# Kernel tuning notes

Measured on AMD Instinct MI355X. Metric: run time of the kernel, lower is better.

Reference implementation:

```python
import jax, jax.numpy as jnp
import numpy as np

V, E, H, L, B = 32000, 128, 32, 64, 32


def setup_inputs() -> dict:
    key = jax.random.key(0)
    k0, k1, k2, k3, k4, k5 = jax.random.split(key, 6)
    stdv = 1.0 / np.sqrt(H)
    we = jax.random.uniform(k0, (V, E), minval=-stdv, maxval=stdv, dtype=jnp.float32)
    we = we.at[1].set(0.0)  # pad token row zeroed, as in original
    i2h1 = jax.random.uniform(k1, (E + H, H), minval=-stdv, maxval=stdv, dtype=jnp.float32)
    i2h2 = jax.random.uniform(k2, (E + H, H), minval=-stdv, maxval=stdv, dtype=jnp.float32)
    h2o = jax.random.uniform(k3, (2 * H, V), minval=-stdv, maxval=stdv, dtype=jnp.float32)
    bias = jnp.ones((1, H), dtype=jnp.float32)  # assigned after reset_parameters -> stays ones
    hidden_init = jax.random.normal(k4, (1, H), dtype=jnp.float32)  # plain buffer, not reset
    inp = jax.random.randint(k5, (L, B), 0, V, dtype=jnp.int64)
    return {"inp": inp, "we": we, "i2h1": i2h1, "i2h2": i2h2,
            "h2o": h2o, "bias": bias, "hidden_init": hidden_init}


def reference(inp, we, i2h1, i2h2, h2o, bias, hidden_init):
    Lr, Br = inp.shape
    Hh = hidden_init.shape[1]
    emb = we[inp]                                   # [L,B,E] embedding gather
    h0 = jnp.broadcast_to(hidden_init, (Br, Hh))    # [B,H]
    b = jnp.broadcast_to(bias, (Br, Hh))            # [B,H]

    def make_step(W):
        def step(h, e):
            h_new = jnp.tanh(jnp.concatenate([e, h], axis=1) @ W + b)
            return h_new, h_new
        return step

    # forward direction: hf[i] = hidden after consuming token i
    _, hf = jax.lax.scan(make_step(i2h1), h0, emb)
    # backward direction (scan over reversed time, flip back)
    _, hb_rev = jax.lax.scan(make_step(i2h2), h0, emb[::-1])
    hb = hb_rev[::-1]                               # hb[i] = bwd hidden after token i

    # original uses hiddenf[i] (pre-token-i fwd state) and hiddenb[i+1] (post-token-(i+1) bwd state)
    hf_used = jnp.concatenate([h0[None], hf[:-1]], axis=0)   # [L,B,H]
    hb_used = jnp.concatenate([hb[1:], h0[None]], axis=0)    # [L,B,H]

    hcat = jnp.concatenate([hf_used, hb_used], axis=-1)      # [L,B,2H]
    logits = jnp.einsum('lbh,hv->lbv', hcat, h2o)            # [L,B,V]
    return jax.nn.log_softmax(logits, axis=-1)
```

## Files before the change

kernel.cpp:

```cpp
#include <hip/hip_runtime.h>
#include <hip/hip_cooperative_groups.h>

namespace cg = cooperative_groups;

#define V_SZ 32000
#define E_SZ 128
#define H_SZ 32
#define L_SZ 64
#define B_SZ 32
#define M_TOT 2048
#define K2 64
#define NVT 125

typedef __bf16 bf16x8 __attribute__((ext_vector_type(8)));
typedef float f32x4 __attribute__((ext_vector_type(4)));

__device__ __forceinline__ unsigned short f2bf(float f) {
    unsigned int u = __float_as_uint(f);
    u += 0x7FFFu + ((u >> 16) & 1u);
    return (unsigned short)(u >> 16);
}

__device__ __forceinline__ void load_vfrag(
    const __bf16* __restrict__ h2oT, int vbase, int lg, int lr,
    bf16x8 vf[4][2]) {
#pragma unroll
    for (int i = 0; i < 4; ++i) {
        const __bf16* vp = h2oT + (size_t)(vbase + i * 16 + lr) * K2 + lg * 8;
        vf[i][0] = *(const bf16x8*)(vp);
        vf[i][1] = *(const bf16x8*)(vp + 32);
    }
}

__device__ __forceinline__ void load_hfrag(
    const __bf16* __restrict__ hcat, int rowbase, int lg, int lr,
    bf16x8 hf[4][2]) {
#pragma unroll
    for (int j = 0; j < 4; ++j) {
        const __bf16* hp = hcat + (size_t)(rowbase + j * 16 + lr) * K2 + lg * 8;
        hf[j][0] = *(const bf16x8*)(hp);
        hf[j][1] = *(const bf16x8*)(hp + 32);
    }
}

__device__ __forceinline__ void tile_gemm_t(
    const bf16x8 vf[4][2], const bf16x8 hf[4][2], f32x4 acc[4][4]) {
#pragma unroll
    for (int i = 0; i < 4; ++i)
#pragma unroll
        for (int j = 0; j < 4; ++j) acc[i][j] = (f32x4){0.f, 0.f, 0.f, 0.f};
#pragma unroll
    for (int i = 0; i < 4; ++i)
#pragma unroll
        for (int j = 0; j < 4; ++j) {
            acc[i][j] = __builtin_amdgcn_mfma_f32_16x16x32_bf16(vf[i][0], hf[j][0], acc[i][j], 0, 0, 0);
            acc[i][j] = __builtin_amdgcn_mfma_f32_16x16x32_bf16(vf[i][1], hf[j][1], acc[i][j], 0, 0, 0);
        }
}

template <typename EP>
__device__ __forceinline__ void sweep8(
    const __bf16* __restrict__ hcat, int y0, int lg, int lr, EP&& ep) {
    bf16x8 hfA[4][2], hfB[4][2];
    load_hfrag(hcat, y0, lg, lr, hfA);
#pragma unroll
    for (int t = 0; t < 8; ++t) {
        if (t & 1) {
            if (t < 7) load_hfrag(hcat, y0 + (t + 1) * 64, lg, lr, hfA);
            ep(hfB, y0 + t * 64);
        } else {
            if (t < 7) load_hfrag(hcat, y0 + (t + 1) * 64, lg, lr, hfB);
            ep(hfA, y0 + t * 64);
        }
    }
}

struct EpA {
    const bf16x8 (*vf)[2];
    float* S;
    int lane, lg, lr;
    __device__ __forceinline__ void operator()(const bf16x8 hf[4][2], int rowbase) const {
        f32x4 acc[4][4];
        tile_gemm_t((const bf16x8(*)[2])vf, hf, acc);
        float srow[4];
#pragma unroll
        for (int j = 0; j < 4; ++j) {
            float s = 0.f;
#pragma unroll
            for (int i = 0; i < 4; ++i)
#pragma unroll
                for (int r = 0; r < 4; ++r) s += __expf(acc[i][j][r]);
            srow[j] = s;
        }
#pragma unroll
        for (int j = 0; j < 4; ++j) {
            srow[j] += __shfl_xor(srow[j], 16, 64);
            srow[j] += __shfl_xor(srow[j], 32, 64);
        }
        if (lane < 16) {
#pragma unroll
            for (int j = 0; j < 4; ++j)
                atomicAdd(&S[rowbase + j * 16 + lane], srow[j]);
        }
    }
};

struct EpB {
    const bf16x8 (*vf)[2];
    const float* S;
    float* out;
    int vbase, lg, lr;
    __device__ __forceinline__ void operator()(const bf16x8 hf[4][2], int rowbase) const {
        float lsev[4];
#pragma unroll
        for (int j = 0; j < 4; ++j)
            lsev[j] = logf(S[rowbase + j * 16 + lr]);
        f32x4 acc[4][4];
        tile_gemm_t((const bf16x8(*)[2])vf, hf, acc);
#pragma unroll
        for (int j = 0; j < 4; ++j) {
            float* rp = out + (size_t)(rowbase + j * 16 + lr) * V_SZ + vbase + lg * 4;
#pragma unroll
            for (int i = 0; i < 4; ++i) {
                f32x4 v;
                v.x = acc[i][j].x - lsev[j];
                v.y = acc[i][j].y - lsev[j];
                v.z = acc[i][j].z - lsev[j];
                v.w = acc[i][j].w - lsev[j];
                *(f32x4*)(rp + i * 16) = v;
            }
        }
    }
};

__global__ __launch_bounds__(256) void k_prep_rnn(
    const int* __restrict__ inp, const float* __restrict__ we,
    const float* __restrict__ i2h1, const float* __restrict__ i2h2,
    const float* __restrict__ h2o, const float* __restrict__ bias,
    const float* __restrict__ hinit,
    unsigned short* __restrict__ hcat_u, unsigned short* __restrict__ h2oT_u,
    float* __restrict__ S) {
    const int tid = threadIdx.x;
    const int p = blockIdx.x;
    if (p < 500) {
        if (p == 0) {
#pragma unroll
            for (int i = tid; i < M_TOT; i += 256) S[i] = 0.f;
        }
        const int v = p * 64 + (tid & 63);
        const int kg = tid >> 6;
        unsigned int* dst = (unsigned int*)(h2oT_u + (size_t)v * K2 + kg * 16);
#pragma unroll
        for (int kk = 0; kk < 16; kk += 2) {
            const int k = kg * 16 + kk;
            float a = h2o[(size_t)k * V_SZ + v];
            float b = h2o[(size_t)(k + 1) * V_SZ + v];
            dst[kk >> 1] = (unsigned int)f2bf(a) | ((unsigned int)f2bf(b) << 16);
        }
        return;
    }
    const int w2 = p - 500;
    const int dir = w2 >> 4;
    const int bpair = w2 & 15;
    const float* W = dir ? i2h2 : i2h1;
    __shared__ float Xl[L_SZ * 2 * H_SZ];
    {
        const int j = tid & 31, bb = (tid >> 5) & 1, to = tid >> 6;
        const int b = bpair * 2 + bb;
        const float bj = bias[j];
        for (int tt = 0; tt < 16; ++tt) {
            const int t = to * 16 + tt;
            const int idx = inp[t * B_SZ + b];
            const float* er = we + (size_t)idx * E_SZ;
            float acc = bj;
#pragma unroll
            for (int k0 = 0; k0 < E_SZ; k0 += 4) {
                f32x4 e4 = *(const f32x4*)(er + k0);
                acc += e4.x * W[(k0 + 0) * H_SZ + j];
                acc += e4.y * W[(k0 + 1) * H_SZ + j];
                acc += e4.z * W[(k0 + 2) * H_SZ + j];
                acc += e4.w * W[(k0 + 3) * H_SZ + j];
            }
            Xl[(t * 2 + bb) * H_SZ + j] = acc;
        }
    }
    __syncthreads();
    if (tid < 64) {
        const int lane = tid;
        const int bb = lane >> 5;
        const int b = bpair * 2 + bb;
        const int j = lane & 31;
        const int srcbase = lane & 32;
        float wh[H_SZ];
#pragma unroll
        for (int k = 0; k < H_SZ; ++k) wh[k] = W[(E_SZ + k) * H_SZ + j];
        float h = hinit[j];
        for (int step = 0; step < L_SZ; ++step) {
            const int tt = dir ? (L_SZ - 1 - step) : step;
            hcat_u[(tt * B_SZ + b) * K2 + dir * H_SZ + j] = f2bf(h);
            float a0 = Xl[(tt * 2 + bb) * H_SZ + j];
            float a1 = 0.f, a2 = 0.f, a3 = 0.f;
#pragma unroll
            for (int k = 0; k < H_SZ; k += 4) {
                a0 += __shfl(h, srcbase | k, 64) * wh[k];
                a1 += __shfl(h, srcbase | (k + 1), 64) * wh[k + 1];
                a2 += __shfl(h, srcbase | (k + 2), 64) * wh[k + 2];
                a3 += __shfl(h, srcbase | (k + 3), 64) * wh[k + 3];
            }
            float x2 = (a0 + a1) + (a2 + a3);
            float e = __expf(2.f * x2);
            h = 1.f - 2.f * __builtin_amdgcn_rcpf(e + 1.f);
        }
    }
}

__global__ __launch_bounds__(256) void k_fused(
    const unsigned short* __restrict__ hcat_u,
    const unsigned short* __restrict__ h2oT_u,
    float* __restrict__ S, float* __restrict__ out) {
    cg::grid_group gg = cg::this_grid();
    const int tid = threadIdx.x;
    const int wave = tid >> 6, lane = tid & 63;
    const int lg = lane >> 4, lr = lane & 15;
    const int xcol = blockIdx.x >> 2;
    const int y0 = (blockIdx.x & 3) * 512;
    const int vbase = xcol * 256 + wave * 64;
    const __bf16* hcat = (const __bf16*)hcat_u;
    const __bf16* h2oT = (const __bf16*)h2oT_u;

    bf16x8 vf[4][2];
    load_vfrag(h2oT, vbase, lg, lr, vf);

    EpA epa{vf, S, lane, lg, lr};
    sweep8(hcat, y0, lg, lr, epa);

    __threadfence();
    gg.sync();

    EpB epb{vf, S, out, vbase, lg, lr};
    sweep8(hcat, y0, lg, lr, epb);
}

__global__ __launch_bounds__(256) void k_pass_a(
    const __bf16* __restrict__ hcat, const __bf16* __restrict__ h2oT,
    float* __restrict__ S) {
    const int tid = threadIdx.x;
    const int wave = tid >> 6, lane = tid & 63;
    const int lg = lane >> 4, lr = lane & 15;
    const int y0 = blockIdx.y * 512;
    const int vbase = blockIdx.x * 256 + wave * 64;
    bf16x8 vf[4][2];
    load_vfrag(h2oT, vbase, lg, lr, vf);
    EpA epa{vf, S, lane, lg, lr};
    sweep8(hcat, y0, lg, lr, epa);
}

__global__ __launch_bounds__(256) void k_pass_b(
    const __bf16* __restrict__ hcat, const __bf16* __restrict__ h2oT,
    const float* __restrict__ S, float* __restrict__ out) {
    const int tid = threadIdx.x;
    const int wave = tid >> 6, lane = tid & 63;
    const int lg = lane >> 4, lr = lane & 15;
    const int y0 = blockIdx.y * 512;
    const int vbase = blockIdx.x * 256 + wave * 64;
    bf16x8 vf[4][2];
    load_vfrag(h2oT, vbase, lg, lr, vf);
    EpB epb{vf, S, out, vbase, lg, lr};
    sweep8(hcat, y0, lg, lr, epb);
}

extern "C" void kernel_launch(void* const* d_in, const int* in_sizes, int n_in,
                              void* d_out, int out_size, void* d_ws, size_t ws_size,
                              hipStream_t stream) {
    (void)in_sizes; (void)n_in; (void)out_size; (void)ws_size;
    const int*   inp   = (const int*)d_in[0];
    const float* we    = (const float*)d_in[1];
    const float* i2h1  = (const float*)d_in[2];
    const float* i2h2  = (const float*)d_in[3];
    const float* h2o   = (const float*)d_in[4];
    const float* bias  = (const float*)d_in[5];
    const float* hinit = (const float*)d_in[6];
    float* out = (float*)d_out;
    char* ws = (char*)d_ws;
    unsigned short* hcat_u = (unsigned short*)(ws);
    unsigned short* h2oT_u = (unsigned short*)(ws + 262144);
    float*          S      = (float*)(ws + 4358144);

    k_prep_rnn<<<532, 256, 0, stream>>>(inp, we, i2h1, i2h2, h2o, bias, hinit,
                                        hcat_u, h2oT_u, S);

    hipError_t e = hipErrorUnknown;
    int occ = 0;
    if (hipOccupancyMaxActiveBlocksPerMultiprocessor(&occ, k_fused, 256, 0)
            == hipSuccess && occ * 256 >= 500) {
        void* args[] = {(void*)&hcat_u, (void*)&h2oT_u, (void*)&S, (void*)&out};
        e = hipLaunchCooperativeKernel((void*)k_fused, dim3(500), dim3(256),
                                       args, 0, stream);
    }
    if (e != hipSuccess) {
        k_pass_a<<<dim3(NVT, 4), 256, 0, stream>>>(
            (const __bf16*)hcat_u, (const __bf16*)h2oT_u, S);
        k_pass_b<<<dim3(NVT, 4), 256, 0, stream>>>(
            (const __bf16*)hcat_u, (const __bf16*)h2oT_u, S, out);
    }
}
```

Before: 154.1 us.

## Fold prep/RNN into cooperative kernel and double grid with half-height row tiles

Moves the h2o transpose, RNN recurrence and S zeroing into the cooperative fused kernel behind an extra grid sync, removing a separate kernel launch. It also doubles the cooperative grid to 1000 blocks (launch_bounds 256,4), with each block sweeping 256 rows instead of 512, which spreads the GEMM and log-softmax work over more CUs. In exchange there is one more grid-wide barrier, the serial RNN blocks now sit on the critical path inside the fused kernel, and each block reloads its h2o fragments for half as much reuse.

```diff
diff --git a/kernel.cpp b/kernel.cpp
--- a/kernel.cpp
+++ b/kernel.cpp
@@ -11,6 +11,7 @@
 #define M_TOT 2048
 #define K2 64
 #define NVT 125
+#define GRID_F 1000
 
 typedef __bf16 bf16x8 __attribute__((ext_vector_type(8)));
 typedef float f32x4 __attribute__((ext_vector_type(4)));
@@ -59,26 +60,23 @@
 }
 
 template <typename EP>
-__device__ __forceinline__ void sweep8(
+__device__ __forceinline__ void sweep4(
     const __bf16* __restrict__ hcat, int y0, int lg, int lr, EP&& ep) {
     bf16x8 hfA[4][2], hfB[4][2];
     load_hfrag(hcat, y0, lg, lr, hfA);
-#pragma unroll
-    for (int t = 0; t < 8; ++t) {
-        if (t & 1) {
-            if (t < 7) load_hfrag(hcat, y0 + (t + 1) * 64, lg, lr, hfA);
-            ep(hfB, y0 + t * 64);
-        } else {
-            if (t < 7) load_hfrag(hcat, y0 + (t + 1) * 64, lg, lr, hfB);
-            ep(hfA, y0 + t * 64);
-        }
-    }
+    load_hfrag(hcat, y0 + 64, lg, lr, hfB);
+    ep(hfA, y0);
+    load_hfrag(hcat, y0 + 128, lg, lr, hfA);
+    ep(hfB, y0 + 64);
+    load_hfrag(hcat, y0 + 192, lg, lr, hfB);
+    ep(hfA, y0 + 128);
+    ep(hfB, y0 + 192);
 }
 
 struct EpA {
     const bf16x8 (*vf)[2];
     float* S;
-    int lane, lg, lr;
+    int lane;
     __device__ __forceinline__ void operator()(const bf16x8 hf[4][2], int rowbase) const {
         f32x4 acc[4][4];
         tile_gemm_t((const bf16x8(*)[2])vf, hf, acc);
@@ -133,37 +131,29 @@
     }
 };
 
-__global__ __launch_bounds__(256) void k_prep_rnn(
-    const int* __restrict__ inp, const float* __restrict__ we,
-    const float* __restrict__ i2h1, const float* __restrict__ i2h2,
-    const float* __restrict__ h2o, const float* __restrict__ bias,
-    const float* __restrict__ hinit,
-    unsigned short* __restrict__ hcat_u, unsigned short* __restrict__ h2oT_u,
-    float* __restrict__ S) {
-    const int tid = threadIdx.x;
-    const int p = blockIdx.x;
-    if (p < 500) {
-        if (p == 0) {
-#pragma unroll
-            for (int i = tid; i < M_TOT; i += 256) S[i] = 0.f;
-        }
-        const int v = p * 64 + (tid & 63);
-        const int kg = tid >> 6;
-        unsigned int* dst = (unsigned int*)(h2oT_u + (size_t)v * K2 + kg * 16);
-#pragma unroll
-        for (int kk = 0; kk < 16; kk += 2) {
-            const int k = kg * 16 + kk;
-            float a = h2o[(size_t)k * V_SZ + v];
-            float b = h2o[(size_t)(k + 1) * V_SZ + v];
-            dst[kk >> 1] = (unsigned int)f2bf(a) | ((unsigned int)f2bf(b) << 16);
-        }
-        return;
-    }
-    const int w2 = p - 500;
+__device__ __forceinline__ void transpose_unit(
+    int p, int tid, const float* __restrict__ h2o,
+    unsigned short* __restrict__ h2oT_u) {
+    const int v = p * 64 + (tid & 63);
+    const int kg = tid >> 6;
+    unsigned int* dst = (unsigned int*)(h2oT_u + (size_t)v * K2 + kg * 16);
+#pragma unroll
+    for (int kk = 0; kk < 16; kk += 2) {
+        const int k = kg * 16 + kk;
+        float a = h2o[(size_t)k * V_SZ + v];
+        float b = h2o[(size_t)(k + 1) * V_SZ + v];
+        dst[kk >> 1] = (unsigned int)f2bf(a) | ((unsigned int)f2bf(b) << 16);
+    }
+}
+
+__device__ __forceinline__ void rnn_unit(
+    int w2, int tid, float* Xl, const int* __restrict__ inp,
+    const float* __restrict__ we, const float* __restrict__ i2h1,
+    const float* __restrict__ i2h2, const float* __restrict__ bias,
+    const float* __restrict__ hinit, unsigned short* __restrict__ hcat_u) {
     const int dir = w2 >> 4;
     const int bpair = w2 & 15;
     const float* W = dir ? i2h2 : i2h1;
-    __shared__ float Xl[L_SZ * 2 * H_SZ];
     {
         const int j = tid & 31, bb = (tid >> 5) & 1, to = tid >> 6;
         const int b = bpair * 2 + bb;
@@ -214,31 +204,65 @@
     }
 }
 
-__global__ __launch_bounds__(256) void k_fused(
-    const unsigned short* __restrict__ hcat_u,
-    const unsigned short* __restrict__ h2oT_u,
+__global__ __launch_bounds__(256, 4) void k_fused(
+    const int* __restrict__ inp, const float* __restrict__ we,
+    const float* __restrict__ i2h1, const float* __restrict__ i2h2,
+    const float* __restrict__ h2o, const float* __restrict__ bias,
+    const float* __restrict__ hinit,
+    unsigned short* __restrict__ hcat_u, unsigned short* __restrict__ h2oT_u,
     float* __restrict__ S, float* __restrict__ out) {
     cg::grid_group gg = cg::this_grid();
+    __shared__ float Xl[L_SZ * 2 * H_SZ];
     const int tid = threadIdx.x;
+    const int p = blockIdx.x;
     const int wave = tid >> 6, lane = tid & 63;
     const int lg = lane >> 4, lr = lane & 15;
-    const int xcol = blockIdx.x >> 2;
-    const int y0 = (blockIdx.x & 3) * 512;
-    const int vbase = xcol * 256 + wave * 64;
+
+    if (p < 500) {
+        transpose_unit(p, tid, h2o, h2oT_u);
+    } else if (p < 532) {
+        rnn_unit(p - 500, tid, Xl, inp, we, i2h1, i2h2, bias, hinit, hcat_u);
+    } else if (p == 532) {
+        for (int i = tid; i < M_TOT; i += 256) S[i] = 0.f;
+    }
+    __threadfence();
+    gg.sync();
+
     const __bf16* hcat = (const __bf16*)hcat_u;
     const __bf16* h2oT = (const __bf16*)h2oT_u;
+    const int xcol = p >> 3;
+    const int y0 = (p & 7) * 256;
+    const int vbase = xcol * 256 + wave * 64;
 
     bf16x8 vf[4][2];
     load_vfrag(h2oT, vbase, lg, lr, vf);
 
-    EpA epa{vf, S, lane, lg, lr};
-    sweep8(hcat, y0, lg, lr, epa);
-
+    EpA epa{vf, S, lane};
+    sweep4(hcat, y0, lg, lr, epa);
     __threadfence();
     gg.sync();
 
     EpB epb{vf, S, out, vbase, lg, lr};
-    sweep8(hcat, y0, lg, lr, epb);
+    sweep4(hcat, y0, lg, lr, epb);
+}
+
+__global__ __launch_bounds__(256) void k_prep_rnn(
+    const int* __restrict__ inp, const float* __restrict__ we,
+    const float* __restrict__ i2h1, const float* __restrict__ i2h2,
+    const float* __restrict__ h2o, const float* __restrict__ bias,
+    const float* __restrict__ hinit,
+    unsigned short* __restrict__ hcat_u, unsigned short* __restrict__ h2oT_u,
+    float* __restrict__ S) {
+    __shared__ float Xl[L_SZ * 2 * H_SZ];
+    const int tid = threadIdx.x;
+    const int p = blockIdx.x;
+    if (p < 500) {
+        if (p == 0)
+            for (int i = tid; i < M_TOT; i += 256) S[i] = 0.f;
+        transpose_unit(p, tid, h2o, h2oT_u);
+        return;
+    }
+    rnn_unit(p - 500, tid, Xl, inp, we, i2h1, i2h2, bias, hinit, hcat_u);
 }
 
 __global__ __launch_bounds__(256) void k_pass_a(
@@ -247,12 +271,12 @@
     const int tid = threadIdx.x;
     const int wave = tid >> 6, lane = tid & 63;
     const int lg = lane >> 4, lr = lane & 15;
-    const int y0 = blockIdx.y * 512;
+    const int y0 = blockIdx.y * 256;
     const int vbase = blockIdx.x * 256 + wave * 64;
     bf16x8 vf[4][2];
     load_vfrag(h2oT, vbase, lg, lr, vf);
-    EpA epa{vf, S, lane, lg, lr};
-    sweep8(hcat, y0, lg, lr, epa);
+    EpA epa{vf, S, lane};
+    sweep4(hcat, y0, lg, lr, epa);
 }
 
 __global__ __launch_bounds__(256) void k_pass_b(
@@ -261,12 +285,12 @@
     const int tid = threadIdx.x;
     const int wave = tid >> 6, lane = tid & 63;
     const int lg = lane >> 4, lr = lane & 15;
-    const int y0 = blockIdx.y * 512;
+    const int y0 = blockIdx.y * 256;
     const int vbase = blockIdx.x * 256 + wave * 64;
     bf16x8 vf[4][2];
     load_vfrag(h2oT, vbase, lg, lr, vf);
     EpB epb{vf, S, out, vbase, lg, lr};
-    sweep8(hcat, y0, lg, lr, epb);
+    sweep4(hcat, y0, lg, lr, epb);
 }
 
 extern "C" void kernel_launch(void* const* d_in, const int* in_sizes, int n_in,
@@ -286,21 +310,23 @@
     unsigned short* h2oT_u = (unsigned short*)(ws + 262144);
     float*          S      = (float*)(ws + 4358144);
 
-    k_prep_rnn<<<532, 256, 0, stream>>>(inp, we, i2h1, i2h2, h2o, bias, hinit,
-                                        hcat_u, h2oT_u, S);
-
     hipError_t e = hipErrorUnknown;
     int occ = 0;
     if (hipOccupancyMaxActiveBlocksPerMultiprocessor(&occ, k_fused, 256, 0)
-            == hipSuccess && occ * 256 >= 500) {
-        void* args[] = {(void*)&hcat_u, (void*)&h2oT_u, (void*)&S, (void*)&out};
-        e = hipLaunchCooperativeKernel((void*)k_fused, dim3(500), dim3(256),
+            == hipSuccess && occ * 256 >= GRID_F) {
+        void* args[] = {
+            (void*)&inp, (void*)&we, (void*)&i2h1, (void*)&i2h2, (void*)&h2o,
+            (void*)&bias, (void*)&hinit, (void*)&hcat_u, (void*)&h2oT_u,
+            (void*)&S, (void*)&out};
+        e = hipLaunchCooperativeKernel((void*)k_fused, dim3(GRID_F), dim3(256),
                                        args, 0, stream);
     }
     if (e != hipSuccess) {
-        k_pass_a<<<dim3(NVT, 4), 256, 0, stream>>>(
+        k_prep_rnn<<<532, 256, 0, stream>>>(inp, we, i2h1, i2h2, h2o, bias,
+                                            hinit, hcat_u, h2oT_u, S);
+        k_pass_a<<<dim3(NVT, 8), 256, 0, stream>>>(
             (const __bf16*)hcat_u, (const __bf16*)h2oT_u, S);
-        k_pass_b<<<dim3(NVT, 4), 256, 0, stream>>>(
+        k_pass_b<<<dim3(NVT, 8), 256, 0, stream>>>(
             (const __bf16*)hcat_u, (const __bf16*)h2oT_u, S, out);
     }
 }
```

Result: slower. 158.5 us (+2.9%).
